# Performance work log

Measured on AMD Instinct MI355X. Metric: run time of the kernel, lower is better.

## Reference

```python
import jax, jax.numpy as jnp
import numpy as np

IUNITS = 64  # input channels; scale is sqrt(iunits), per the original code


def setup_inputs() -> dict:
    key = jax.random.key(0)
    ks = jax.random.split(key, 4)
    B, N, Cin, Cout = 16, 2048, 64, 128
    x = jax.random.normal(ks[0], (B, N, Cin), dtype=jnp.float32)
    # 0.05 scaling keeps naive exp/sum softmax in a sane numeric range
    Wq = jax.random.normal(ks[1], (Cin, Cout), dtype=jnp.float32) * 0.05
    Wk = jax.random.normal(ks[2], (Cin, Cout), dtype=jnp.float32) * 0.05
    Wv = jax.random.normal(ks[3], (Cin, Cout), dtype=jnp.float32) * 0.05
    bq = jnp.zeros((Cout,), dtype=jnp.float32)
    bk = jnp.zeros((Cout,), dtype=jnp.float32)
    bv = jnp.zeros((Cout,), dtype=jnp.float32)
    return {"x": x, "Wq": Wq, "bq": bq, "Wk": Wk, "bk": bk, "Wv": Wv, "bv": bv}


def reference(x, Wq, bq, Wk, bk, Wv, bv):
    # Dense projections with ReLU activation (as in the original Dense(..., activation='relu'))
    Q = jax.nn.relu(jnp.einsum('bnc,cd->bnd', x, Wq) + bq)  # [B,N,D]
    K = jax.nn.relu(jnp.einsum('bnc,cd->bnd', x, Wk) + bk)  # [B,N,D]
    V = jax.nn.relu(jnp.einsum('bnc,cd->bnd', x, Wv) + bv)  # [B,N,D]
    scale = jnp.sqrt(jnp.float32(IUNITS))  # NOTE: sqrt of INPUT units, per source
    qk = jnp.einsum('bnd,bmd->bnm', Q, K) / scale            # [B,N,N]
    # exp/sum softmax over last axis; jax.nn.softmax is the same math, stabilized
    wgts = jax.nn.softmax(qk, axis=-1)
    return jnp.einsum('bnm,bmd->bnd', wgts, V)               # [B,N,D]
```

## Files before the change

kernel.cpp:

```cpp
#include <hip/hip_runtime.h>

typedef unsigned short u16;
typedef unsigned int u32;
typedef __bf16 bf16x8 __attribute__((ext_vector_type(8)));
typedef float f32x16 __attribute__((ext_vector_type(16)));
typedef u32 u32x4 __attribute__((ext_vector_type(4)));

#define QSCALE 0.18033688011112042f

__device__ __forceinline__ u16 bfbits(float f) {
  __bf16 h = (__bf16)f;
  return __builtin_bit_cast(u16, h);
}
__device__ __forceinline__ u32 pack2(float lo, float hi) {
  return (u32)bfbits(lo) | ((u32)bfbits(hi) << 16);
}
__device__ __forceinline__ void pl32swap(u32& a, u32& b) {
  asm volatile("v_permlane32_swap_b32 %0, %1" : "+v"(a), "+v"(b));
}
__device__ __forceinline__ void gload_lds16(const void* g, void* l) {
  __builtin_amdgcn_global_load_lds(
      (const __attribute__((address_space(1))) void*)g,
      (__attribute__((address_space(3))) void*)l, 16, 0, 0);
}

__global__ __launch_bounds__(256) void proj_kernel(
    const float* __restrict__ x,
    const float* __restrict__ Wq, const float* __restrict__ bq,
    const float* __restrict__ Wk, const float* __restrict__ bk,
    const float* __restrict__ Wv, const float* __restrict__ bv,
    u16* __restrict__ Qb, u16* __restrict__ Kb, u16* __restrict__ VbT) {
  __shared__ __align__(16) u16 xs[64 * 64];
  const int t = threadIdx.x, w = t >> 6, lane = t & 63;
  const int ql = lane & 31, hi = lane >> 5;
  const int ws_ = w & 1;
  const int th = w >> 1;
  const size_t rg0 = (size_t)blockIdx.x * 64;

  {
    const float4* xsrc = reinterpret_cast<const float4*>(x + rg0 * 64);
#pragma unroll
    for (int i = 0; i < 4; ++i) {
      int idx = t + i * 256;
      int row = idx >> 4, c4 = idx & 15;
      float4 v = xsrc[idx];
      char* p = reinterpret_cast<char*>(xs) + row * 128 + ((c4 * 8) ^ ((row & 7) << 4));
      *reinterpret_cast<uint2*>(p) = make_uint2(pack2(v.x, v.y), pack2(v.z, v.w));
    }
  }
  __syncthreads();

  bf16x8 xf[4];
  {
    const int row = ws_ * 32 + ql;
    const char* base = reinterpret_cast<const char*>(xs) + row * 128;
    const int swz = (row & 7) << 4;
#pragma unroll
    for (int j = 0; j < 4; ++j)
      xf[j] = *reinterpret_cast<const bf16x8*>(base + ((j * 32 + hi * 16) ^ swz));
  }

  const float* Wm[3] = {Wq, Wk, Wv};
  const float* bmm[3] = {bq, bk, bv};
  const int b = (int)(rg0 >> 11);
  const int n0 = (int)(rg0 & 2047);

#pragma unroll
  for (int tl6 = 0; tl6 < 6; ++tl6) {
    const int tl = th * 6 + tl6;
    const int m = tl >> 2, ct = tl & 3;
    const float* W = Wm[m];
    const int c = ct * 32 + ql;
    f32x16 acc;
#pragma unroll
    for (int i2 = 0; i2 < 16; ++i2) acc[i2] = 0.f;
#pragma unroll
    for (int j = 0; j < 4; ++j) {
      u32 wp[4];
#pragma unroll
      for (int e2 = 0; e2 < 4; ++e2) {
        float w0 = W[(j * 16 + hi * 8 + 2 * e2) * 128 + c];
        float w1 = W[(j * 16 + hi * 8 + 2 * e2 + 1) * 128 + c];
        wp[e2] = pack2(w0, w1);
      }
      u32x4 ww; ww.x = wp[0]; ww.y = wp[1]; ww.z = wp[2]; ww.w = wp[3];
      const bf16x8 wf = __builtin_bit_cast(bf16x8, ww);
      acc = __builtin_amdgcn_mfma_f32_32x32x16_bf16(xf[j], wf, acc, 0, 0, 0);
    }
    const float bias = bmm[m][c];
    if (m == 0) {
#pragma unroll
      for (int reg = 0; reg < 16; ++reg) {
        const int i = (reg & 3) + 8 * (reg >> 2) + 4 * hi;
        Qb[(rg0 + ws_ * 32 + i) * 128 + c] =
            bfbits(fmaxf(acc[reg] + bias, 0.f) * QSCALE);
      }
    } else if (m == 1) {
#pragma unroll
      for (int reg = 0; reg < 16; ++reg) {
        const int i = (reg & 3) + 8 * (reg >> 2) + 4 * hi;
        Kb[(rg0 + ws_ * 32 + i) * 128 + c] = bfbits(fmaxf(acc[reg] + bias, 0.f));
      }
    } else {
      u16* vrow = VbT + ((size_t)(b * 128 + c)) * 2048;
#pragma unroll
      for (int g2 = 0; g2 < 4; ++g2) {
        u32 p0 = pack2(fmaxf(acc[4 * g2 + 0] + bias, 0.f),
                       fmaxf(acc[4 * g2 + 1] + bias, 0.f));
        u32 p1 = pack2(fmaxf(acc[4 * g2 + 2] + bias, 0.f),
                       fmaxf(acc[4 * g2 + 3] + bias, 0.f));
        const int n = n0 + ws_ * 32 + 8 * g2 + 4 * hi;
        *reinterpret_cast<uint2*>(vrow + n) = make_uint2(p0, p1);
      }
    }
  }
}

__global__ __launch_bounds__(256) void attn_kernel(
    const u16* __restrict__ Qb, const u16* __restrict__ Kb,
    const u16* __restrict__ VbT, float* __restrict__ out) {
  __shared__ __align__(16) char smem[65536];

  const int bid = ((int)blockIdx.x & 7) * 64 + ((int)blockIdx.x >> 3);
  const int b = bid >> 5;
  const int qt = bid & 31;
  const int t = threadIdx.x, w = t >> 6, lane = t & 63;
  const int qw = w >> 1, par = w & 1;
  const int ql = lane & 31, hi = lane >> 5;
  const int q0 = qt * 64 + qw * 32;
  const int sw = (ql & 7) << 4;

  bf16x8 qf[8];
  const u16* Qrow = Qb + ((size_t)(b * 2048 + q0 + ql)) * 128;
#pragma unroll
  for (int f = 0; f < 8; ++f)
    qf[f] = *reinterpret_cast<const bf16x8*>(Qrow + f * 16 + hi * 8);

  f32x16 Oacc[4], lacc;
#pragma unroll
  for (int i = 0; i < 16; ++i) {
    Oacc[0][i] = 0.f; Oacc[1][i] = 0.f; Oacc[2][i] = 0.f; Oacc[3][i] = 0.f;
    lacc[i] = 0.f;
  }
  u32x4 ow; ow.x = ow.y = ow.z = ow.w = 0x3F803F80u;
  const bf16x8 ones = __builtin_bit_cast(bf16x8, ow);

  const u16* Kbase = Kb + (size_t)b * 2048 * 128;
  const u16* Vbase = VbT + (size_t)b * 128 * 2048;

  const u16* kgp[4]; const u16* vgp[4];
  int ldso[4];
#pragma unroll
  for (int i = 0; i < 4; ++i) {
    const int Lb = (w * 4 + i) * 1024 + lane * 16;
    ldso[i] = (w * 4 + i) * 1024;
    const int kr = Lb >> 8;
    const int ks = ((Lb >> 4) & 15) ^ (kr & 7);
    kgp[i] = Kbase + kr * 128 + ks * 8;
    const int vr = Lb >> 7;
    const int vs = ((Lb >> 4) & 7) ^ (vr & 7);
    vgp[i] = Vbase + (size_t)vr * 2048 + vs * 8;
  }

#pragma unroll
  for (int i = 0; i < 4; ++i) {
    gload_lds16(kgp[i], smem + ldso[i]);
    gload_lds16(vgp[i], smem + 32768 + ldso[i]);
  }
  __syncthreads();

  for (int ss = 0; ss < 32; ++ss) {
    const int cur = ss & 1;
    if (ss < 31) {
      const size_t ko = (size_t)(ss + 1) * 8192;
      const int vo = (ss + 1) * 64;
      const int bo = (cur ^ 1) * 16384;
#pragma unroll
      for (int i = 0; i < 4; ++i) {
        gload_lds16(kgp[i] + ko, smem + bo + ldso[i]);
        gload_lds16(vgp[i] + vo, smem + 32768 + bo + ldso[i]);
      }
    }
    const char* kb0 = smem + cur * 16384;
    const char* vb0 = smem + 32768 + cur * 16384;

    f32x16 s0;
#pragma unroll
    for (int i = 0; i < 16; ++i) s0[i] = 0.f;
    const char* kbp = kb0 + (par * 32 + ql) * 256;
    __builtin_amdgcn_s_setprio(1);
#pragma unroll
    for (int f = 0; f < 8; ++f) {
      bf16x8 k0 = *reinterpret_cast<const bf16x8*>(kbp + ((f * 32 + hi * 16) ^ sw));
      s0 = __builtin_amdgcn_mfma_f32_32x32x16_bf16(k0, qf[f], s0, 0, 0, 0);
    }
    __builtin_amdgcn_s_setprio(0);

    u32 pk[8];
#pragma unroll
    for (int m = 0; m < 8; ++m)
      pk[m] = pack2(__builtin_amdgcn_exp2f(s0[2 * m]),
                    __builtin_amdgcn_exp2f(s0[2 * m + 1]));

    __builtin_amdgcn_s_setprio(1);
#pragma unroll
    for (int s2 = 0; s2 < 2; ++s2) {
      u32 X0 = pk[4 * s2 + 0], X1 = pk[4 * s2 + 1];
      u32 Y0 = pk[4 * s2 + 2], Y1 = pk[4 * s2 + 3];
      pl32swap(X0, Y0);
      pl32swap(X1, Y1);
      u32x4 frw; frw.x = X0; frw.y = X1; frw.z = Y0; frw.w = Y1;
      const bf16x8 pf = __builtin_bit_cast(bf16x8, frw);
      lacc = __builtin_amdgcn_mfma_f32_32x32x16_bf16(pf, ones, lacc, 0, 0, 0);
#pragma unroll
      for (int dt = 0; dt < 4; ++dt) {
        const int dr = dt * 32 + ql;
        bf16x8 vf = *reinterpret_cast<const bf16x8*>(
            vb0 + dr * 128 + ((par * 64 + s2 * 32 + hi * 16) ^ ((dr & 7) << 4)));
        Oacc[dt] = __builtin_amdgcn_mfma_f32_32x32x16_bf16(pf, vf, Oacc[dt], 0, 0, 0);
      }
    }
    __builtin_amdgcn_s_setprio(0);

    __syncthreads();
  }

  float* Ost = reinterpret_cast<float*>(smem);
  float* Lst = reinterpret_cast<float*>(smem + 32768);
  if (par == 1) {
#pragma unroll
    for (int reg = 0; reg < 16; ++reg) {
      const int qr = (reg & 3) + 8 * (reg >> 2) + 4 * hi;
      float* orow = Ost + (size_t)(qw * 32 + qr) * 128 + ql;
#pragma unroll
      for (int dt = 0; dt < 4; ++dt) orow[dt * 32] = Oacc[dt][reg];
      if (ql == 0) Lst[qw * 32 + qr] = lacc[reg];
    }
  }
  __syncthreads();
  if (par == 0) {
#pragma unroll
    for (int reg = 0; reg < 16; ++reg) {
      const int qr = (reg & 3) + 8 * (reg >> 2) + 4 * hi;
      const float inv = 1.f / (lacc[reg] + Lst[qw * 32 + qr]);
      const float* prow = Ost + (size_t)(qw * 32 + qr) * 128 + ql;
      float* orow = out + ((size_t)(b * 2048 + q0 + qr)) * 128 + ql;
#pragma unroll
      for (int dt = 0; dt < 4; ++dt)
        orow[dt * 32] = (Oacc[dt][reg] + prow[dt * 32]) * inv;
    }
  }
}

extern "C" void kernel_launch(void* const* d_in, const int* in_sizes, int n_in,
                              void* d_out, int out_size, void* d_ws, size_t ws_size,
                              hipStream_t stream) {
  const float* x  = (const float*)d_in[0];
  const float* Wq = (const float*)d_in[1];
  const float* bq = (const float*)d_in[2];
  const float* Wk = (const float*)d_in[3];
  const float* bk = (const float*)d_in[4];
  const float* Wv = (const float*)d_in[5];
  const float* bv = (const float*)d_in[6];
  float* out = (float*)d_out;

  u16* Qb  = (u16*)d_ws;
  u16* Kb  = Qb + (size_t)16 * 2048 * 128;
  u16* VbT = Kb + (size_t)16 * 2048 * 128;

  proj_kernel<<<512, 256, 0, stream>>>(x, Wq, bq, Wk, bk, Wv, bv, Qb, Kb, VbT);
  attn_kernel<<<512, 256, 0, stream>>>(Qb, Kb, VbT, out);
}
```

Baseline: 72.44 us.

## Fuse Q projection into attention kernel, keep projected Q in LDS

After: 70.26 us. 3.0% less time.

```diff
diff --git a/kernel.cpp b/kernel.cpp
--- a/kernel.cpp
+++ b/kernel.cpp
@@ -24,12 +24,11 @@
       (__attribute__((address_space(3))) void*)l, 16, 0, 0);
 }
 
-__global__ __launch_bounds__(256) void proj_kernel(
+__global__ __launch_bounds__(256) void kv_proj_kernel(
     const float* __restrict__ x,
-    const float* __restrict__ Wq, const float* __restrict__ bq,
     const float* __restrict__ Wk, const float* __restrict__ bk,
     const float* __restrict__ Wv, const float* __restrict__ bv,
-    u16* __restrict__ Qb, u16* __restrict__ Kb, u16* __restrict__ VbT) {
+    u16* __restrict__ Kb, u16* __restrict__ VbT) {
   __shared__ __align__(16) u16 xs[64 * 64];
   const int t = threadIdx.x, w = t >> 6, lane = t & 63;
   const int ql = lane & 31, hi = lane >> 5;
@@ -60,16 +59,13 @@
       xf[j] = *reinterpret_cast<const bf16x8*>(base + ((j * 32 + hi * 16) ^ swz));
   }
 
-  const float* Wm[3] = {Wq, Wk, Wv};
-  const float* bmm[3] = {bq, bk, bv};
+  const float* W = th ? Wv : Wk;
+  const float* bb = th ? bv : bk;
   const int b = (int)(rg0 >> 11);
   const int n0 = (int)(rg0 & 2047);
 
 #pragma unroll
-  for (int tl6 = 0; tl6 < 6; ++tl6) {
-    const int tl = th * 6 + tl6;
-    const int m = tl >> 2, ct = tl & 3;
-    const float* W = Wm[m];
+  for (int ct = 0; ct < 4; ++ct) {
     const int c = ct * 32 + ql;
     f32x16 acc;
 #pragma unroll
@@ -87,15 +83,8 @@
       const bf16x8 wf = __builtin_bit_cast(bf16x8, ww);
       acc = __builtin_amdgcn_mfma_f32_32x32x16_bf16(xf[j], wf, acc, 0, 0, 0);
     }
-    const float bias = bmm[m][c];
-    if (m == 0) {
-#pragma unroll
-      for (int reg = 0; reg < 16; ++reg) {
-        const int i = (reg & 3) + 8 * (reg >> 2) + 4 * hi;
-        Qb[(rg0 + ws_ * 32 + i) * 128 + c] =
-            bfbits(fmaxf(acc[reg] + bias, 0.f) * QSCALE);
-      }
-    } else if (m == 1) {
+    const float bias = bb[c];
+    if (th == 0) {
 #pragma unroll
       for (int reg = 0; reg < 16; ++reg) {
         const int i = (reg & 3) + 8 * (reg >> 2) + 4 * hi;
@@ -117,24 +106,87 @@
 }
 
 __global__ __launch_bounds__(256) void attn_kernel(
-    const u16* __restrict__ Qb, const u16* __restrict__ Kb,
-    const u16* __restrict__ VbT, float* __restrict__ out) {
+    const float* __restrict__ x,
+    const float* __restrict__ Wq, const float* __restrict__ bq,
+    const u16* __restrict__ Kb, const u16* __restrict__ VbT,
+    float* __restrict__ out) {
   __shared__ __align__(16) char smem[65536];
 
   const int bid = ((int)blockIdx.x & 7) * 64 + ((int)blockIdx.x >> 3);
   const int b = bid >> 5;
   const int qt = bid & 31;
   const int t = threadIdx.x, w = t >> 6, lane = t & 63;
+  const int ql = lane & 31, hi = lane >> 5;
+  const size_t rg0 = (size_t)b * 2048 + qt * 64;
+  const int sw = (ql & 7) << 4;
+
+  {
+    u16* xs = reinterpret_cast<u16*>(smem + 16384);
+    const float4* xsrc = reinterpret_cast<const float4*>(x + rg0 * 64);
+#pragma unroll
+    for (int i = 0; i < 4; ++i) {
+      int idx = t + i * 256;
+      int row = idx >> 4, c4 = idx & 15;
+      float4 v = xsrc[idx];
+      char* p = reinterpret_cast<char*>(xs) + row * 128 + ((c4 * 8) ^ ((row & 7) << 4));
+      *reinterpret_cast<uint2*>(p) = make_uint2(pack2(v.x, v.y), pack2(v.z, v.w));
+    }
+    __syncthreads();
+
+    const int ws_ = w & 1;
+    bf16x8 xf[4];
+    {
+      const int row = ws_ * 32 + ql;
+      const char* base = reinterpret_cast<const char*>(xs) + row * 128;
+      const int swz = (row & 7) << 4;
+#pragma unroll
+      for (int j = 0; j < 4; ++j)
+        xf[j] = *reinterpret_cast<const bf16x8*>(base + ((j * 32 + hi * 16) ^ swz));
+    }
+#pragma unroll
+    for (int u = 0; u < 2; ++u) {
+      const int ct = (w >> 1) * 2 + u;
+      const int c = ct * 32 + ql;
+      f32x16 acc;
+#pragma unroll
+      for (int i2 = 0; i2 < 16; ++i2) acc[i2] = 0.f;
+#pragma unroll
+      for (int j = 0; j < 4; ++j) {
+        u32 wp[4];
+#pragma unroll
+        for (int e2 = 0; e2 < 4; ++e2) {
+          float w0 = Wq[(j * 16 + hi * 8 + 2 * e2) * 128 + c];
+          float w1 = Wq[(j * 16 + hi * 8 + 2 * e2 + 1) * 128 + c];
+          wp[e2] = pack2(w0, w1);
+        }
+        u32x4 ww; ww.x = wp[0]; ww.y = wp[1]; ww.z = wp[2]; ww.w = wp[3];
+        const bf16x8 wf = __builtin_bit_cast(bf16x8, ww);
+        acc = __builtin_amdgcn_mfma_f32_32x32x16_bf16(xf[j], wf, acc, 0, 0, 0);
+      }
+      const float bias = bq[c];
+#pragma unroll
+      for (int reg = 0; reg < 16; ++reg) {
+        const int i = (reg & 3) + 8 * (reg >> 2) + 4 * hi;
+        const int r = ws_ * 32 + i;
+        *reinterpret_cast<u16*>(smem + r * 256 + ((2 * c) ^ ((r & 7) << 4))) =
+            bfbits(fmaxf(acc[reg] + bias, 0.f) * QSCALE);
+      }
+    }
+  }
+  __syncthreads();
+
   const int qw = w >> 1, par = w & 1;
-  const int ql = lane & 31, hi = lane >> 5;
   const int q0 = qt * 64 + qw * 32;
-  const int sw = (ql & 7) << 4;
-
   bf16x8 qf[8];
-  const u16* Qrow = Qb + ((size_t)(b * 2048 + q0 + ql)) * 128;
-#pragma unroll
-  for (int f = 0; f < 8; ++f)
-    qf[f] = *reinterpret_cast<const bf16x8*>(Qrow + f * 16 + hi * 8);
+  {
+    const int r = qw * 32 + ql;
+    const char* base = smem + r * 256;
+    const int swz = (r & 7) << 4;
+#pragma unroll
+    for (int f = 0; f < 8; ++f)
+      qf[f] = *reinterpret_cast<const bf16x8*>(base + ((f * 32 + hi * 16) ^ swz));
+  }
+  __syncthreads();
 
   f32x16 Oacc[4], lacc;
 #pragma unroll
@@ -264,10 +316,9 @@
   const float* bv = (const float*)d_in[6];
   float* out = (float*)d_out;
 
-  u16* Qb  = (u16*)d_ws;
-  u16* Kb  = Qb + (size_t)16 * 2048 * 128;
+  u16* Kb  = (u16*)d_ws;
   u16* VbT = Kb + (size_t)16 * 2048 * 128;
 
-  proj_kernel<<<512, 256, 0, stream>>>(x, Wq, bq, Wk, bk, Wv, bv, Qb, Kb, VbT);
-  attn_kernel<<<512, 256, 0, stream>>>(Qb, Kb, VbT, out);
-}
+  kv_proj_kernel<<<512, 256, 0, stream>>>(x, Wk, bk, Wv, bv, Kb, VbT);
+  attn_kernel<<<512, 256, 0, stream>>>(x, Wq, bq, Kb, VbT, out);
+}
```
